# Kernel tuning notes

Measured on AMD Instinct MI355X. Metric: run time of the kernel, lower is better.

## Reference

```python
import jax, jax.numpy as jnp
import numpy as np

D_MODEL = 1024
NUM_HEADS = 16
HEAD_DIM = D_MODEL // NUM_HEADS


def setup_inputs() -> dict:
    key = jax.random.key(0)
    ks = jax.random.split(key, 11)
    B, S, D = 2, 2048, D_MODEL
    scale = 1.0 / np.sqrt(D)
    inp = {
        "q": jax.random.normal(ks[0], (B, S, D), dtype=jnp.float32),
        "k": jax.random.normal(ks[1], (B, S, D), dtype=jnp.float32),
        "v": jax.random.normal(ks[2], (B, S, D), dtype=jnp.float32),
        # torch nn.Linear weights are [out, in]; y = x @ W.T + b
        "Wq": jax.random.normal(ks[3], (D, D), dtype=jnp.float32) * scale,
        "bq": jnp.zeros((D,), dtype=jnp.float32),
        "Wk": jax.random.normal(ks[4], (D, D), dtype=jnp.float32) * scale,
        "bk": jnp.zeros((D,), dtype=jnp.float32),
        "Wv": jax.random.normal(ks[5], (D, D), dtype=jnp.float32) * scale,
        "bv": jnp.zeros((D,), dtype=jnp.float32),
        "Wo": jax.random.normal(ks[6], (D, D), dtype=jnp.float32) * scale,
        "bo": jnp.zeros((D,), dtype=jnp.float32),
    }
    return inp


def _split_heads(x):
    B, S, D = x.shape
    return x.reshape(B, S, NUM_HEADS, HEAD_DIM).transpose(0, 2, 1, 3)  # [B,H,S,hd]


def reference(q, k, v, Wq, bq, Wk, bk, Wv, bv, Wo, bo):
    B, S, D = q.shape
    qh = _split_heads(q @ Wq.T + bq)
    kh = _split_heads(k @ Wk.T + bk)
    vh = _split_heads(v @ Wv.T + bv)
    # scores: [B,H,S,S], causal mask, softmax
    scores = jnp.einsum("bhqd,bhkd->bhqk", qh, kh) / jnp.sqrt(
        jnp.asarray(HEAD_DIM, dtype=qh.dtype))
    causal = jnp.tril(jnp.ones((S, S), dtype=bool))
    scores = jnp.where(causal[None, None], scores, -jnp.inf)
    attn = jax.nn.softmax(scores, axis=-1)
    out = jnp.einsum("bhqk,bhkd->bhqd", attn, vh)  # [B,H,S,hd]
    out = out.transpose(0, 2, 1, 3).reshape(B, S, D)
    return out @ Wo.T + bo
```

## Files before the change

### kernel.cpp

```cpp
#include <hip/hip_runtime.h>
#include <hip/hip_bf16.h>
#include <cstdint>
#include <cstddef>

typedef __bf16 bf16;
typedef __bf16 bf16x2 __attribute__((ext_vector_type(2)));
typedef __bf16 bf16x4 __attribute__((ext_vector_type(4)));
typedef __bf16 bf16x8 __attribute__((ext_vector_type(8)));
typedef float f32x4 __attribute__((ext_vector_type(4)));
typedef float f32x16 __attribute__((ext_vector_type(16)));
typedef unsigned int u32x4 __attribute__((ext_vector_type(4)));

#define S_LEN 2048
#define DM 1024
#define NH 16
#define HD 64
#define NQKV (4096 * 1024)
#define NW (1024 * 1024)
#define QK_SCALE 0.18033688011112042f

__device__ __forceinline__ void gload_lds16(const bf16* g, bf16* l) {
  __builtin_amdgcn_global_load_lds(
      (const __attribute__((address_space(1))) void*)g,
      (__attribute__((address_space(3))) void*)l, 16, 0, 0);
}

__device__ __forceinline__ unsigned packbf(float lo, float hi) {
  bf16x2 t;
  t[0] = (bf16)lo;
  t[1] = (bf16)hi;
  return __builtin_bit_cast(unsigned, t);
}

__device__ __forceinline__ void pl32swap(unsigned& a, unsigned& b) {
#if __has_builtin(__builtin_amdgcn_permlane32_swap)
  auto r = __builtin_amdgcn_permlane32_swap((int)a, (int)b, false, false);
  a = (unsigned)r[0];
  b = (unsigned)r[1];
#else
  asm volatile("v_permlane32_swap_b32 %0, %1" : "+v"(a), "+v"(b));
#endif
}

__global__ __launch_bounds__(256) void cvt_all(
    const float* __restrict__ q, const float* __restrict__ k, const float* __restrict__ v,
    const float* __restrict__ Wq, const float* __restrict__ Wk, const float* __restrict__ Wv,
    const float* __restrict__ Wo, bf16* __restrict__ out) {
  const size_t i = ((size_t)blockIdx.x * 256 + threadIdx.x) * 8;
  const float* src;
  size_t off;
  if (i < (size_t)NQKV) { src = q; off = i; }
  else if (i < 2ull * NQKV) { src = k; off = i - NQKV; }
  else if (i < 3ull * NQKV) { src = v; off = i - 2ull * NQKV; }
  else {
    const size_t j = i - 3ull * NQKV;
    if (j < (size_t)NW) { src = Wq; off = j; }
    else if (j < 2ull * NW) { src = Wk; off = j - NW; }
    else if (j < 3ull * NW) { src = Wv; off = j - 2ull * NW; }
    else { src = Wo; off = j - 3ull * NW; }
  }
  const float4 a = *(const float4*)(src + off);
  const float4 b = *(const float4*)(src + off + 4);
  bf16x8 o;
  o[0] = (bf16)a.x; o[1] = (bf16)a.y; o[2] = (bf16)a.z; o[3] = (bf16)a.w;
  o[4] = (bf16)b.x; o[5] = (bf16)b.y; o[6] = (bf16)b.z; o[7] = (bf16)b.w;
  *(bf16x8*)(out + i) = o;
}

template <int MODE>
__global__ __launch_bounds__(256, 2) void gemm_bt(
    const bf16* __restrict__ A, const bf16* __restrict__ W,
    const float* __restrict__ bias0, const float* __restrict__ bias1,
    const float* __restrict__ bias2, void* __restrict__ Out,
    int M, int N, int K, float scale) {
  __shared__ __align__(16) bf16 sm[2 * 128 * 64];
  bf16* Asl = sm;
  bf16* Bsl = sm + 128 * 64;
  const int tid = threadIdx.x;
  const int lane = tid & 63, w = tid >> 6;
  const int wr = w >> 1, wc = w & 1;
  const int r16 = lane & 15, grp = lane >> 4;

  int flat = blockIdx.y * gridDim.x + blockIdx.x;
  const int cpx = (gridDim.x * gridDim.y) >> 3;
  flat = (flat & 7) * cpx + (flat >> 3);
  const int m0 = (flat / gridDim.x) * 128;
  const int n0 = (flat % gridDim.x) * 128;

  const int seg = n0 >> 10;
  const bf16* Ab = (MODE == 3) ? A + (size_t)seg * NQKV : A;

  f32x4 acc[4][4] = {};

  const int nk = K >> 6;
  for (int t = 0; t < nk; ++t) {
    const int k0 = t << 6;
    __syncthreads();
#pragma unroll
    for (int j = 0; j < 4; ++j) {
      const int lin = j * 256 + tid;
      const int rr = lin >> 3;
      const int cc = (lin & 7) * 8;
      gload_lds16(&Ab[(size_t)(m0 + rr) * K + k0 + cc], &Asl[lin * 8]);
      gload_lds16(&W[(size_t)(n0 + rr) * K + k0 + cc], &Bsl[lin * 8]);
    }
    __syncthreads();
#pragma unroll
    for (int kk = 0; kk < 2; ++kk) {
      bf16x8 af[4], bfr[4];
#pragma unroll
      for (int m = 0; m < 4; ++m)
        af[m] = *(const bf16x8*)&Asl[(wr * 64 + m * 16 + r16) * 64 + kk * 32 + grp * 8];
#pragma unroll
      for (int n = 0; n < 4; ++n)
        bfr[n] = *(const bf16x8*)&Bsl[(wc * 64 + n * 16 + r16) * 64 + kk * 32 + grp * 8];
#pragma unroll
      for (int m = 0; m < 4; ++m)
#pragma unroll
        for (int n = 0; n < 4; ++n)
          acc[m][n] = __builtin_amdgcn_mfma_f32_16x16x32_bf16(af[m], bfr[n], acc[m][n], 0, 0, 0);
    }
  }

  const float* bp = (MODE == 3) ? (seg == 0 ? bias0 : (seg == 1 ? bias1 : bias2)) : bias0;
  const float sc = (MODE == 3) ? (seg == 0 ? scale : 1.0f) : scale;

  if (MODE == 3 && seg == 2) {
    __syncthreads();
    bf16* T = sm + w * (32 * 76);
    const int b = (m0 + wr * 64) >> 11;
    const int srow0 = (m0 + wr * 64) & 2047;
    bf16* base2 = (bf16*)Out + 2 * (size_t)NQKV;
#pragma unroll
    for (int p = 0; p < 2; ++p) {
#pragma unroll
      for (int nn = 0; nn < 2; ++nn) {
        const int n = 2 * p + nn;
#pragma unroll
        for (int mq = 0; mq < 4; ++mq)
#pragma unroll
          for (int r = 0; r < 4; ++r) {
            const int d_l = nn * 16 + r16;
            const int s_l = mq * 16 + grp * 4 + r;
            const int cs = (n0 + wc * 64 + n * 16 + r16) & 1023;
            T[d_l * 76 + s_l] = (bf16)(acc[mq][n][r] + bp[cs]);
          }
      }
      __syncthreads();
#pragma unroll
      for (int j = 0; j < 4; ++j) {
        const int d_l = j * 8 + (lane >> 3);
        const int scnk = lane & 7;
        const uint2 lo = *(const uint2*)&T[d_l * 76 + scnk * 8];
        const uint2 hi = *(const uint2*)&T[d_l * 76 + scnk * 8 + 4];
        const int cs = (n0 + wc * 64 + p * 32 + d_l) & 1023;
        const int hh = cs >> 6, dd = cs & 63;
        bf16* dst = base2 + ((size_t)(b * NH + hh) * HD + dd) * S_LEN + srow0 + scnk * 8;
        uint4 val; val.x = lo.x; val.y = lo.y; val.z = hi.x; val.w = hi.y;
        *(uint4*)dst = val;
      }
      __syncthreads();
    }
    return;
  }

#pragma unroll
  for (int m = 0; m < 4; ++m) {
#pragma unroll
    for (int n = 0; n < 4; ++n) {
#pragma unroll
      for (int r = 0; r < 4; ++r) {
        const int row = m0 + wr * 64 + m * 16 + grp * 4 + r;
        const int col = n0 + wc * 64 + n * 16 + r16;
        const int cs = col & 1023;
        const float v = (acc[m][n][r] + bp[cs]) * sc;
        if (MODE == 3) {
          const int b = row >> 11, s = row & 2047, h = cs >> 6, d = cs & 63;
          bf16* base = (bf16*)Out + (size_t)seg * NQKV;
          base[((size_t)(b * NH + h) * S_LEN + s) * HD + d] = (bf16)v;
        } else {
          ((float*)Out)[(size_t)row * N + col] = v;
        }
      }
    }
  }
}

__global__ __launch_bounds__(256, 2) void attn_fwd8(
    const bf16* __restrict__ Qh, const bf16* __restrict__ Kh,
    const bf16* __restrict__ Vt, bf16* __restrict__ AO) {
  __shared__ __align__(16) bf16 Kl[3][64 * 64];
  __shared__ __align__(16) bf16 Vl[3][64 * 64];

  const int tid = threadIdx.x;
  const int lane = tid & 63, w = tid >> 6;
  const int q31 = lane & 31, h = lane >> 5;
  const int qh = w >> 1, kh = w & 1;
  const int koff = kh << 5;

  const int bid = blockIdx.x;
  const int xcd = bid & 7;
  const int within = bid >> 3;
  const int bh = xcd * 4 + (within & 3);
  const int p = within >> 2;

  const bf16* Qb = Qh + (size_t)bh * S_LEN * HD;
  const bf16* Kb = Kh + (size_t)bh * S_LEN * HD;
  const bf16* Vb = Vt + (size_t)bh * HD * S_LEN;

  int stK[2], stV[2], stL[2];
#pragma unroll
  for (int i = 0; i < 2; ++i) {
    const int lin = i * 256 + tid;
    const int row = lin >> 3;
    const int colb = (lin & 7) * 16;
    const int scol = colb ^ ((row & 7) << 4);
    stK[i] = row * HD + (scol >> 1);
    stV[i] = row * S_LEN + (scol >> 1);
    stL[i] = lin * 8;
  }
  const int swz = (q31 & 7) << 4;

#define STAGE(t, buf)                                                          \
  {                                                                            \
    const bf16* kb_ = Kb + (size_t)(t) * 64 * HD;                              \
    const bf16* vb_ = Vb + (t) * 64;                                           \
    _Pragma("unroll") for (int i = 0; i < 2; ++i) {                            \
      gload_lds16(kb_ + stK[i], &Kl[buf][stL[i]]);                             \
      gload_lds16(vb_ + stV[i], &Vl[buf][stL[i]]);                             \
    }                                                                          \
  }

  auto run_chunk = [&](const int q0, const int nt) {
    const int q0w = q0 + (qh << 5);
    const int qg = q0w + q31;
    const int nt_w = (w == 1) ? nt - 1 : nt;
    const bool maskw = (w == 0) || (w == 3);

    bf16x8 qf[4];
#pragma unroll
    for (int ks = 0; ks < 4; ++ks)
      qf[ks] = *(const bf16x8*)&Qb[(size_t)qg * HD + ks * 16 + 8 * h];

    f32x16 acc0 = {}, acc1 = {};
    float m = -1e30f, l = 0.f;

    STAGE(0, 0)
    STAGE(1, 1)

    int cur = 0;
    for (int kt = 0; kt < nt; ++kt) {
      if (kt + 1 < nt) asm volatile("s_waitcnt vmcnt(4)" ::: "memory");
      else             asm volatile("s_waitcnt vmcnt(0)" ::: "memory");
      __builtin_amdgcn_s_barrier();

      if (kt + 2 < nt) {
        int nxt = cur + 2; if (nxt >= 3) nxt -= 3;
        STAGE(kt + 2, nxt)
      }

      if (kt < nt_w) {
        const bf16* KlC = &Kl[cur][0];
        const bf16* VlC = &Vl[cur][0];

        bf16x8 kf[4];
#pragma unroll
        for (int ks = 0; ks < 4; ++ks) {
          const int c = (32 * ks + 16 * h) ^ swz;
          kf[ks] = *(const bf16x8*)((const char*)KlC + (koff + q31) * 128 + c);
        }

        f32x16 p0 = {};
        __builtin_amdgcn_s_setprio(1);
#pragma unroll
        for (int ks = 0; ks < 4; ++ks)
          p0 = __builtin_amdgcn_mfma_f32_32x32x16_bf16(kf[ks], qf[ks], p0, 0, 0, 0);
        __builtin_amdgcn_s_setprio(0);

        bf16x8 vf[4];
#pragma unroll
        for (int ks = 0; ks < 2; ++ks)
#pragma unroll
          for (int db = 0; db < 2; ++db) {
            const int c = (64 * kh + 32 * ks + 16 * h) ^ swz;
            vf[ks * 2 + db] =
                *(const bf16x8*)((const char*)VlC + (db * 32 + q31) * 128 + c);
          }

        if (maskw && kt == nt - 1) {
#pragma unroll
          for (int r = 0; r < 16; ++r) {
            const int key = (kt << 6) + koff + (r & 3) + 8 * (r >> 2) + 4 * h;
            if (key > qg) p0[r] = -1e30f;
          }
        }
        float t_[16];
#pragma unroll
        for (int r = 0; r < 16; ++r) t_[r] = p0[r];
#pragma unroll
        for (int s = 8; s >= 1; s >>= 1)
#pragma unroll
          for (int r = 0; r < s; ++r) t_[r] = fmaxf(t_[r], t_[r + s]);
        const float pmax = fmaxf(t_[0], __shfl_xor(t_[0], 32));
        if (!__all(pmax - m <= 8.0f)) {
          const float mn = fmaxf(m, pmax);
          const float al = exp2f(m - mn);
          m = mn;
          l *= al;
#pragma unroll
          for (int r = 0; r < 16; ++r) { acc0[r] *= al; acc1[r] *= al; }
        }
        float sv[16];
#pragma unroll
        for (int r = 0; r < 16; ++r) {
          p0[r] = exp2f(p0[r] - m);
          sv[r] = p0[r];
        }
#pragma unroll
        for (int s = 8; s >= 1; s >>= 1)
#pragma unroll
          for (int r = 0; r < s; ++r) sv[r] += sv[r + s];
        l += sv[0] + __shfl_xor(sv[0], 32);

        unsigned wv[8];
#pragma unroll
        for (int mm = 0; mm < 8; ++mm)
          wv[mm] = packbf(p0[2 * mm], p0[2 * mm + 1]);
        pl32swap(wv[0], wv[2]);
        pl32swap(wv[1], wv[3]);
        pl32swap(wv[4], wv[6]);
        pl32swap(wv[5], wv[7]);

        __builtin_amdgcn_s_setprio(1);
        {
          u32x4 pu0 = {wv[0], wv[1], wv[2], wv[3]};
          const bf16x8 pf0 = __builtin_bit_cast(bf16x8, pu0);
          acc0 = __builtin_amdgcn_mfma_f32_32x32x16_bf16(vf[0], pf0, acc0, 0, 0, 0);
          acc1 = __builtin_amdgcn_mfma_f32_32x32x16_bf16(vf[1], pf0, acc1, 0, 0, 0);
          u32x4 pu1 = {wv[4], wv[5], wv[6], wv[7]};
          const bf16x8 pf1 = __builtin_bit_cast(bf16x8, pu1);
          acc0 = __builtin_amdgcn_mfma_f32_32x32x16_bf16(vf[2], pf1, acc0, 0, 0, 0);
          acc1 = __builtin_amdgcn_mfma_f32_32x32x16_bf16(vf[3], pf1, acc1, 0, 0, 0);
        }
        __builtin_amdgcn_s_setprio(0);
      }

      ++cur; if (cur == 3) cur = 0;
    }

    float* scr = (float*)&Kl[0][0];
    float* s = scr + (size_t)qh * (64 * 34) + lane * 34;
    __syncthreads();
    if (kh) {
#pragma unroll
      for (int r = 0; r < 16; ++r) { s[r] = acc0[r]; s[16 + r] = acc1[r]; }
      s[32] = m;
      s[33] = l;
    }
    __syncthreads();
    if (!kh) {
      const float m1 = s[32], l1 = s[33];
      const float mn = fmaxf(m, m1);
      const float a0 = exp2f(m - mn), a1 = exp2f(m1 - mn);
      const float linv = 1.0f / (a0 * l + a1 * l1);
      const int b = bh >> 4, hh = bh & 15;
      bf16* orow = AO + ((size_t)(b * S_LEN + qg)) * DM + hh * HD;
#pragma unroll
      for (int mm = 0; mm < 4; ++mm) {
        bf16x4 ov0, ov1;
#pragma unroll
        for (int t2 = 0; t2 < 4; ++t2) {
          ov0[t2] = (bf16)((a0 * acc0[4 * mm + t2] + a1 * s[4 * mm + t2]) * linv);
          ov1[t2] = (bf16)((a0 * acc1[4 * mm + t2] + a1 * s[16 + 4 * mm + t2]) * linv);
        }
        *(bf16x4*)&orow[8 * mm + 4 * h] = ov0;
        *(bf16x4*)&orow[32 + 8 * mm + 4 * h] = ov1;
      }
    }
    __syncthreads();
  };

  run_chunk(p << 6, p + 1);
  run_chunk((31 - p) << 6, 32 - p);
#undef STAGE
}

extern "C" void kernel_launch(void* const* d_in, const int* in_sizes, int n_in,
                              void* d_out, int out_size, void* d_ws, size_t ws_size,
                              hipStream_t stream) {
  const float* q  = (const float*)d_in[0];
  const float* k  = (const float*)d_in[1];
  const float* v  = (const float*)d_in[2];
  const float* Wq = (const float*)d_in[3];
  const float* bq = (const float*)d_in[4];
  const float* Wk = (const float*)d_in[5];
  const float* bk = (const float*)d_in[6];
  const float* Wv = (const float*)d_in[7];
  const float* bv = (const float*)d_in[8];
  const float* Wo = (const float*)d_in[9];
  const float* bo = (const float*)d_in[10];

  const int NTOK = 2 * S_LEN;

  bf16* qb  = (bf16*)d_ws;
  bf16* Wqb = qb + 3 * (size_t)NQKV;
  bf16* Wob = Wqb + 3 * (size_t)NW;
  bf16* Qh  = Wqb + 4 * (size_t)NW;
  bf16* Kh  = Qh + (size_t)NQKV;
  bf16* Vt  = Kh + (size_t)NQKV;
  bf16* AO  = Vt + (size_t)NQKV;

  const int cvt_blocks = (3 * NQKV + 4 * NW) / 8 / 256;
  cvt_all<<<cvt_blocks, 256, 0, stream>>>(q, k, v, Wq, Wk, Wv, Wo, qb);

  gemm_bt<3><<<dim3(3 * DM / 128, NTOK / 128), 256, 0, stream>>>(
      qb, Wqb, bq, bk, bv, Qh, NTOK, 3 * DM, DM, QK_SCALE);

  attn_fwd8<<<dim3(512), 256, 0, stream>>>(Qh, Kh, Vt, AO);

  gemm_bt<2><<<dim3(DM / 128, NTOK / 128), 256, 0, stream>>>(
      AO, Wob, bo, bo, bo, d_out, NTOK, DM, DM, 1.0f);
}
```

Before: 121.3 us.

## Software-pipeline QK^T one tile ahead of softmax/PV in attention with 4 LDS buffers

Restructures the attention inner loop so the QK^T MFMAs for tile kt+1 are issued before the softmax and PV work of tile kt, ping-ponging two score accumulators in a 2x unrolled loop. The LDS ring grows from three to four K/V buffers so the prefetch two tiles ahead does not overwrite data still in use. The aim is to overlap matrix-core work with the exp/max/sum vector work. It costs more LDS and registers, which could hurt occupancy at two blocks per CU. The epilogue scratch layout is also changed to a stride of 33 with l stored in a separate array.

```diff
diff --git a/kernel.cpp b/kernel.cpp
--- a/kernel.cpp
+++ b/kernel.cpp
@@ -186,11 +186,11 @@
   }
 }
 
-__global__ __launch_bounds__(256, 2) void attn_fwd8(
+__global__ __launch_bounds__(256, 2) void attn_fwd9(
     const bf16* __restrict__ Qh, const bf16* __restrict__ Kh,
     const bf16* __restrict__ Vt, bf16* __restrict__ AO) {
-  __shared__ __align__(16) bf16 Kl[3][64 * 64];
-  __shared__ __align__(16) bf16 Vl[3][64 * 64];
+  __shared__ __align__(16) bf16 Kl[4][64 * 64];
+  __shared__ __align__(16) bf16 Vl[4][64 * 64];
 
   const int tid = threadIdx.x;
   const int lane = tid & 63, w = tid >> 6;
@@ -244,59 +244,77 @@
 
     f32x16 acc0 = {}, acc1 = {};
     float m = -1e30f, l = 0.f;
+    f32x16 pA = {}, pB = {};
 
     STAGE(0, 0)
-    STAGE(1, 1)
-
-    int cur = 0;
-    for (int kt = 0; kt < nt; ++kt) {
-      if (kt + 1 < nt) asm volatile("s_waitcnt vmcnt(4)" ::: "memory");
-      else             asm volatile("s_waitcnt vmcnt(0)" ::: "memory");
-      __builtin_amdgcn_s_barrier();
-
-      if (kt + 2 < nt) {
-        int nxt = cur + 2; if (nxt >= 3) nxt -= 3;
-        STAGE(kt + 2, nxt)
-      }
-
-      if (kt < nt_w) {
-        const bf16* KlC = &Kl[cur][0];
-        const bf16* VlC = &Vl[cur][0];
-
-        bf16x8 kf[4];
-#pragma unroll
-        for (int ks = 0; ks < 4; ++ks) {
-          const int c = (32 * ks + 16 * h) ^ swz;
-          kf[ks] = *(const bf16x8*)((const char*)KlC + (koff + q31) * 128 + c);
-        }
-
-        f32x16 p0 = {};
-        __builtin_amdgcn_s_setprio(1);
-#pragma unroll
-        for (int ks = 0; ks < 4; ++ks)
-          p0 = __builtin_amdgcn_mfma_f32_32x32x16_bf16(kf[ks], qf[ks], p0, 0, 0, 0);
-        __builtin_amdgcn_s_setprio(0);
-
+    if (nt > 1) {
+      STAGE(1, 1)
+      asm volatile("s_waitcnt vmcnt(4)" ::: "memory");
+    } else {
+      asm volatile("s_waitcnt vmcnt(0)" ::: "memory");
+    }
+    __builtin_amdgcn_s_barrier();
+    if (0 < nt_w) {
+      bf16x8 kf[4];
+#pragma unroll
+      for (int ks = 0; ks < 4; ++ks) {
+        const int c = (32 * ks + 16 * h) ^ swz;
+        kf[ks] = *(const bf16x8*)((const char*)&Kl[0][0] + (koff + q31) * 128 + c);
+      }
+      __builtin_amdgcn_s_setprio(1);
+#pragma unroll
+      for (int ks = 0; ks < 4; ++ks)
+        pA = __builtin_amdgcn_mfma_f32_32x32x16_bf16(kf[ks], qf[ks], pA, 0, 0, 0);
+      __builtin_amdgcn_s_setprio(0);
+    }
+
+    auto body = [&](const int KT, f32x16& PC, f32x16& PN) {
+      if (KT + 1 < nt) {
+        if (KT + 2 < nt) {
+          STAGE(KT + 2, (KT + 2) & 3)
+          asm volatile("s_waitcnt vmcnt(4)" ::: "memory");
+        } else {
+          asm volatile("s_waitcnt vmcnt(0)" ::: "memory");
+        }
+        __builtin_amdgcn_s_barrier();
+        if (KT + 1 < nt_w) {
+          const char* KlN = (const char*)&Kl[(KT + 1) & 3][0];
+          bf16x8 kf[4];
+#pragma unroll
+          for (int ks = 0; ks < 4; ++ks) {
+            const int c = (32 * ks + 16 * h) ^ swz;
+            kf[ks] = *(const bf16x8*)(KlN + (koff + q31) * 128 + c);
+          }
+          PN = {};
+          __builtin_amdgcn_s_setprio(1);
+#pragma unroll
+          for (int ks = 0; ks < 4; ++ks)
+            PN = __builtin_amdgcn_mfma_f32_32x32x16_bf16(kf[ks], qf[ks], PN, 0, 0, 0);
+          __builtin_amdgcn_s_setprio(0);
+        }
+      }
+
+      if (KT < nt_w) {
+        const char* VlC = (const char*)&Vl[KT & 3][0];
         bf16x8 vf[4];
 #pragma unroll
         for (int ks = 0; ks < 2; ++ks)
 #pragma unroll
           for (int db = 0; db < 2; ++db) {
             const int c = (64 * kh + 32 * ks + 16 * h) ^ swz;
-            vf[ks * 2 + db] =
-                *(const bf16x8*)((const char*)VlC + (db * 32 + q31) * 128 + c);
+            vf[ks * 2 + db] = *(const bf16x8*)(VlC + (db * 32 + q31) * 128 + c);
           }
 
-        if (maskw && kt == nt - 1) {
+        if (maskw && KT == nt - 1) {
 #pragma unroll
           for (int r = 0; r < 16; ++r) {
-            const int key = (kt << 6) + koff + (r & 3) + 8 * (r >> 2) + 4 * h;
-            if (key > qg) p0[r] = -1e30f;
+            const int key = (KT << 6) + koff + (r & 3) + 8 * (r >> 2) + 4 * h;
+            if (key > qg) PC[r] = -1e30f;
           }
         }
         float t_[16];
 #pragma unroll
-        for (int r = 0; r < 16; ++r) t_[r] = p0[r];
+        for (int r = 0; r < 16; ++r) t_[r] = PC[r];
 #pragma unroll
         for (int s = 8; s >= 1; s >>= 1)
 #pragma unroll
@@ -313,8 +331,8 @@
         float sv[16];
 #pragma unroll
         for (int r = 0; r < 16; ++r) {
-          p0[r] = exp2f(p0[r] - m);
-          sv[r] = p0[r];
+          PC[r] = exp2f(PC[r] - m);
+          sv[r] = PC[r];
         }
 #pragma unroll
         for (int s = 8; s >= 1; s >>= 1)
@@ -325,7 +343,7 @@
         unsigned wv[8];
 #pragma unroll
         for (int mm = 0; mm < 8; ++mm)
-          wv[mm] = packbf(p0[2 * mm], p0[2 * mm + 1]);
+          wv[mm] = packbf(PC[2 * mm], PC[2 * mm + 1]);
         pl32swap(wv[0], wv[2]);
         pl32swap(wv[1], wv[3]);
         pl32swap(wv[4], wv[6]);
@@ -344,22 +362,28 @@
         }
         __builtin_amdgcn_s_setprio(0);
       }
-
-      ++cur; if (cur == 3) cur = 0;
-    }
+    };
+
+    int kt = 0;
+    for (; kt + 2 <= nt; kt += 2) {
+      body(kt, pA, pB);
+      body(kt + 1, pB, pA);
+    }
+    if (kt < nt) body(kt, pA, pB);
 
     float* scr = (float*)&Kl[0][0];
-    float* s = scr + (size_t)qh * (64 * 34) + lane * 34;
+    float* s = scr + (size_t)qh * (64 * 33) + lane * 33;
     __syncthreads();
     if (kh) {
 #pragma unroll
       for (int r = 0; r < 16; ++r) { s[r] = acc0[r]; s[16 + r] = acc1[r]; }
       s[32] = m;
-      s[33] = l;
-    }
+    }
+    float* sl = scr + 2 * (64 * 33) + (size_t)qh * 64 + lane;
+    if (kh) *sl = l;
     __syncthreads();
     if (!kh) {
-      const float m1 = s[32], l1 = s[33];
+      const float m1 = s[32], l1 = *sl;
       const float mn = fmaxf(m, m1);
       const float a0 = exp2f(m - mn), a1 = exp2f(m1 - mn);
       const float linv = 1.0f / (a0 * l + a1 * l1);
@@ -416,7 +440,7 @@
   gemm_bt<3><<<dim3(3 * DM / 128, NTOK / 128), 256, 0, stream>>>(
       qb, Wqb, bq, bk, bv, Qh, NTOK, 3 * DM, DM, QK_SCALE);
 
-  attn_fwd8<<<dim3(512), 256, 0, stream>>>(Qh, Kh, Vt, AO);
+  attn_fwd9<<<dim3(512), 256, 0, stream>>>(Qh, Kh, Vt, AO);
 
   gemm_bt<2><<<dim3(DM / 128, NTOK / 128), 256, 0, stream>>>(
       AO, Wob, bo, bo, bo, d_out, NTOK, DM, DM, 1.0f);
```

New measurement: 123.9 us. 1.02x slower.
